# Kernel optimization log

Measured on AMD Instinct MI355X. Metric: run time of the kernel, lower is better.

Reference implementation:

```python
import jax, jax.numpy as jnp
import numpy as np

B, S, D = 2, 2048, 1024
H, HKV, HD = 16, 4, 64
FF = 4096
WINDOW = 1024
EPS = 1e-6


def _rope_tables(seq_len, head_dim, base=10000.0):
    inv_freq = 1.0 / (base ** (np.arange(0, head_dim, 2, dtype=np.float32) / head_dim))
    t = np.arange(seq_len, dtype=np.float32)
    freqs = np.outer(t, inv_freq)                       # [S, HD/2]
    emb = np.concatenate([freqs, freqs], axis=-1)       # [S, HD]
    return jnp.asarray(np.cos(emb)), jnp.asarray(np.sin(emb))


def setup_inputs() -> dict:
    key = jax.random.key(0)
    ks = jax.random.split(key, 16)
    s = lambda fan: 1.0 / np.sqrt(fan)
    cos, sin = _rope_tables(S, HD)
    return {
        "hidden_states": jax.random.normal(ks[0], (B, S, D), jnp.float32),
        "cos": cos, "sin": sin,
        "wq": jax.random.normal(ks[1], (D, H * HD), jnp.float32) * s(D),
        "bq": jnp.zeros((H * HD,), jnp.float32),
        "wk": jax.random.normal(ks[2], (D, HKV * HD), jnp.float32) * s(D),
        "bk": jnp.zeros((HKV * HD,), jnp.float32),
        "wv": jax.random.normal(ks[3], (D, HKV * HD), jnp.float32) * s(D),
        "bv": jnp.zeros((HKV * HD,), jnp.float32),
        "wo": jax.random.normal(ks[4], (H * HD, D), jnp.float32) * s(H * HD),
        "ln1_w": jnp.ones((D,), jnp.float32),
        "ln2_w": jnp.ones((D,), jnp.float32),
        "w_gate": jax.random.normal(ks[5], (D, FF), jnp.float32) * s(D),
        "w_up": jax.random.normal(ks[6], (D, FF), jnp.float32) * s(D),
        "w_down": jax.random.normal(ks[7], (FF, D), jnp.float32) * s(FF),
    }


def _rmsnorm(x, w, eps=EPS):
    var = jnp.mean(x.astype(jnp.float32) ** 2, axis=-1, keepdims=True)
    return (x * jax.lax.rsqrt(var + eps)).astype(x.dtype) * w


def _rotate_half(x):
    x1, x2 = jnp.split(x, 2, axis=-1)
    return jnp.concatenate([-x2, x1], axis=-1)


def reference(hidden_states, cos, sin, wq, bq, wk, bk, wv, bv, wo,
              ln1_w, ln2_w, w_gate, w_up, w_down):
    residual = hidden_states
    h = _rmsnorm(hidden_states, ln1_w)

    # projections -> [B, S, H, HD]
    q = (h @ wq + bq).reshape(B, S, H, HD)
    k = (h @ wk + bk).reshape(B, S, HKV, HD)
    v = (h @ wv + bv).reshape(B, S, HKV, HD)

    # RoPE
    c = cos[None, :, None, :]
    sn = sin[None, :, None, :]
    q = q * c + _rotate_half(q) * sn
    k = k * c + _rotate_half(k) * sn

    # GQA: repeat KV heads to H heads
    groups = H // HKV
    k = jnp.repeat(k, groups, axis=2)  # [B, S, H, HD]
    v = jnp.repeat(v, groups, axis=2)

    # sliding-window causal attention (flex_attention block-mask semantics)
    scale = 1.0 / np.sqrt(HD)
    scores = jnp.einsum("bqhd,bkhd->bhqk", q, k) * scale  # [B, H, S, S]
    i = jnp.arange(S)[:, None]
    j = jnp.arange(S)[None, :]
    mask = (j <= i) & (i - j < WINDOW)
    scores = jnp.where(mask[None, None], scores, jnp.finfo(scores.dtype).min)
    attn = jax.nn.softmax(scores, axis=-1)
    ctx = jnp.einsum("bhqk,bkhd->bqhd", attn, v).reshape(B, S, H * HD)

    h = residual + ctx @ wo

    residual2 = h
    h2 = _rmsnorm(h, ln2_w)
    mlp = (jax.nn.silu(h2 @ w_gate) * (h2 @ w_up)) @ w_down
    return residual2 + mlp
```

## Files before the change

kernel.cpp:

```cpp
#include <hip/hip_runtime.h>
#include <hip/hip_bf16.h>
#include <hip/hip_fp16.h>
#include <math.h>

#define BB 2
#define SS 2048
#define DD 1024
#define HH 16
#define HKVN 4
#define HDIM 64
#define FFD 4096
#define WND 1024
#define EPSF 1e-6f

typedef _Float16 f16;
typedef _Float16 half8 __attribute__((ext_vector_type(8)));
typedef float f32x4 __attribute__((ext_vector_type(4)));
typedef unsigned int u32;

#define GLOAD_LDS(gp, lp)                                                  \
  __builtin_amdgcn_global_load_lds(                                        \
      (const __attribute__((address_space(1))) u32*)(gp),                  \
      (__attribute__((address_space(3))) u32*)(lp), 16, 0, 0)

static __device__ inline u32 pack2(float a, float b) {
  unsigned short ua = __builtin_bit_cast(unsigned short, (f16)a);
  unsigned short ub = __builtin_bit_cast(unsigned short, (f16)b);
  return (u32)ua | ((u32)ub << 16);
}

__global__ __launch_bounds__(256) void prep_weights_kernel(
    const float* __restrict__ wq, const float* __restrict__ wk,
    const float* __restrict__ wv, const float* __restrict__ wo,
    const float* __restrict__ wg, const float* __restrict__ wu,
    const float* __restrict__ wd, const float* __restrict__ bq,
    const float* __restrict__ bk, const float* __restrict__ bv,
    f16* __restrict__ qkvT, f16* __restrict__ woT, f16* __restrict__ Wi,
    f16* __restrict__ wdT, float* __restrict__ biasC) {
  int t = blockIdx.x;
  if (t >= 3712) {
    int i = (t - 3712) * 256 + threadIdx.x;
    if (i < 1024)
      biasC[i] = bq[i];
    else if (i < 1280)
      biasC[i] = bk[i - 1024];
    else if (i < 1536)
      biasC[i] = bv[i - 1280];
    return;
  }
  const float* W;
  f16* Wt;
  int K, N, lt, rmul = 1, radd = 0;
  if (t < 256) {
    W = wq; Wt = qkvT; K = 1024; N = 1024; lt = t;
  } else if (t < 320) {
    W = wk; Wt = qkvT + (size_t)1024 * 1024; K = 1024; N = 256; lt = t - 256;
  } else if (t < 384) {
    W = wv; Wt = qkvT + (size_t)1280 * 1024; K = 1024; N = 256; lt = t - 320;
  } else if (t < 640) {
    W = wo; Wt = woT; K = 1024; N = 1024; lt = t - 384;
  } else if (t < 1664) {
    W = wg; Wt = Wi; K = 1024; N = 4096; lt = t - 640; rmul = 2; radd = 0;
  } else if (t < 2688) {
    W = wu; Wt = Wi; K = 1024; N = 4096; lt = t - 1664; rmul = 2; radd = 1;
  } else {
    W = wd; Wt = wdT; K = 4096; N = 1024; lt = t - 2688;
  }
  int ntx = N >> 6;
  int n0 = (lt % ntx) * 64, k0 = (lt / ntx) * 64;
  __shared__ float tile[64][65];
  int tx = threadIdx.x & 63, tr = threadIdx.x >> 6;
#pragma unroll
  for (int i = 0; i < 16; i++) {
    int r = tr + i * 4;
    tile[r][tx] = W[(size_t)(k0 + r) * N + n0 + tx];
  }
  __syncthreads();
  int kx = (threadIdx.x & 31) * 2;
  int rr = threadIdx.x >> 5;
#pragma unroll
  for (int i = 0; i < 8; i++) {
    int r = rr + i * 8;
    u32 w = pack2(tile[kx][r], tile[kx + 1][r]);
    *(u32*)(Wt + ((size_t)((n0 + r) * rmul + radd)) * K + k0 + kx) = w;
  }
}

__global__ __launch_bounds__(256) void rmsnorm_kernel(
    const float* __restrict__ x, const float* __restrict__ w,
    f16* __restrict__ out) {
  int row = blockIdx.x;
  int tid = threadIdx.x;
  float4 v = ((const float4*)(x + (size_t)row * 1024))[tid];
  float ss = v.x * v.x + v.y * v.y + v.z * v.z + v.w * v.w;
  for (int o = 32; o > 0; o >>= 1) ss += __shfl_down(ss, o, 64);
  __shared__ float red[4];
  int wid = tid >> 6, lane = tid & 63;
  if (lane == 0) red[wid] = ss;
  __syncthreads();
  if (tid == 0)
    red[0] = rsqrtf((red[0] + red[1] + red[2] + red[3]) / 1024.f + EPSF);
  __syncthreads();
  float rs = red[0];
  float4 wv = ((const float4*)w)[tid];
  u32 lo = pack2(v.x * rs * wv.x, v.y * rs * wv.y);
  u32 hi = pack2(v.z * rs * wv.z, v.w * rs * wv.w);
  *(int2*)(out + (size_t)row * 1024 + tid * 4) = make_int2((int)lo, (int)hi);
}

__global__ __launch_bounds__(256) void qkv_gemm(
    const f16* __restrict__ A, const f16* __restrict__ Bt,
    const float* __restrict__ biasC, const float* __restrict__ cos_t,
    const float* __restrict__ sin_t, f16* __restrict__ Qh,
    f16* __restrict__ Kh, f16* __restrict__ Vh, int M, int N, int K) {
  __shared__ __align__(16) char smem[3 * 16384];
  const int tid = threadIdx.x;
  const int lane = tid & 63;
  const int wid = tid >> 6;
  const int wr = wid >> 1, wc = wid & 1;
  const int row0 = blockIdx.y * 128, col0 = blockIdx.x * 128;

  f32x4 acc[4][4];
#pragma unroll
  for (int m = 0; m < 4; m++)
#pragma unroll
    for (int n = 0; n < 4; n++) acc[m][n] = (f32x4){0.f, 0.f, 0.f, 0.f};

  auto stage = [&](int buf, int k0) {
    char* base = smem + buf * 16384;
#pragma unroll
    for (int q = 0; q < 2; q++) {
      int s = wid * 128 + q * 64 + lane;
      int r = s >> 2;
      int cg = (s & 3) ^ ((r >> 1) & 3);
      size_t goff = (size_t)r * K + k0 + cg * 8;
      u32 ldsb = (u32)((wid * 2 + q) * 1024);
      GLOAD_LDS(A + (size_t)row0 * K + goff, base + ldsb);
      GLOAD_LDS(Bt + (size_t)col0 * K + goff, base + 8192 + ldsb);
    }
  };
  auto off = [&](int r, int g) -> int {
    return r * 64 + ((g ^ ((r >> 1) & 3)) << 4);
  };

  const int nt = K / 32;
  stage(0, 0);
  if (nt > 1) stage(1, 32);
  int cur = 0;
  const int g = lane >> 4, l15 = lane & 15;
  for (int t = 0; t < nt; t++) {
    if (t + 1 < nt)
      asm volatile("s_waitcnt vmcnt(4)" ::: "memory");
    else
      asm volatile("s_waitcnt vmcnt(0)" ::: "memory");
    asm volatile("s_waitcnt lgkmcnt(0)" ::: "memory");
    __builtin_amdgcn_sched_barrier(0);
    __builtin_amdgcn_s_barrier();
    __builtin_amdgcn_sched_barrier(0);
    const char* base = smem + cur * 16384;
    half8 af[4], bf[4];
#pragma unroll
    for (int m = 0; m < 4; m++) {
      int r = wr * 64 + m * 16 + l15;
      af[m] = *(const half8*)(base + off(r, g));
    }
#pragma unroll
    for (int n = 0; n < 4; n++) {
      int c = wc * 64 + n * 16 + l15;
      bf[n] = *(const half8*)(base + 8192 + off(c, g));
    }
    if (t + 2 < nt) {
      int nb = cur + 2;
      if (nb >= 3) nb -= 3;
      stage(nb, (t + 2) * 32);
    }
    __builtin_amdgcn_s_setprio(1);
#pragma unroll
    for (int m = 0; m < 4; m++)
#pragma unroll
      for (int n = 0; n < 4; n++)
        acc[m][n] =
            __builtin_amdgcn_mfma_f32_16x16x32_f16(af[m], bf[n], acc[m][n], 0, 0, 0);
    __builtin_amdgcn_s_setprio(0);
    cur = (cur + 1 == 3) ? 0 : cur + 1;
  }

  const int typ = (col0 < 1024) ? 0 : (col0 < 1280 ? 1 : 2);
#pragma unroll
  for (int m = 0; m < 4; m++) {
#pragma unroll
    for (int v = 0; v < 4; v++) {
      int r = row0 + wr * 64 + m * 16 + (lane >> 4) * 4 + v;
      int s = r & (SS - 1);
      if (typ == 2) {
#pragma unroll
        for (int n = 0; n < 4; n++) {
          int c = col0 + wc * 64 + n * 16 + l15;
          float vv = acc[m][n][v] + biasC[c];
          Vh[(size_t)r * 256 + (c - 1280)] = (f16)vv;
        }
      } else {
#pragma unroll
        for (int n = 0; n < 2; n++) {
          int d = n * 16 + l15;
          int c1 = col0 + wc * 64 + d;
          float x1 = acc[m][n][v] + biasC[c1];
          float x2 = acc[m][n + 2][v] + biasC[c1 + 32];
          float cv = cos_t[s * HDIM + d];
          float sv = sin_t[s * HDIM + d];
          float o1 = x1 * cv - x2 * sv;
          float o2 = x2 * cv + x1 * sv;
          if (typ == 0) {
            int h = c1 >> 6;
            f16* qp = Qh + ((size_t)r * HH + h) * HDIM + d;
            qp[0] = (f16)(o1 * 0.125f);
            qp[32] = (f16)(o2 * 0.125f);
          } else {
            int hk = (c1 - 1024) >> 6;
            f16* kp = Kh + ((size_t)r * HKVN + hk) * HDIM + d;
            kp[0] = (f16)o1;
            kp[32] = (f16)o2;
          }
        }
      }
    }
  }
}

__global__ __launch_bounds__(256) void gemm_n64(
    const f16* __restrict__ A, const f16* __restrict__ Bt,
    const float* __restrict__ resid, float* __restrict__ Cf, int M, int N,
    int K) {
  __shared__ __align__(16) char smem[3 * 12288];
  const int tid = threadIdx.x;
  const int lane = tid & 63;
  const int wid = tid >> 6;
  const int wr = wid >> 1, wc = wid & 1;
  const int row0 = blockIdx.y * 128, col0 = blockIdx.x * 64;

  f32x4 acc[4][2];
#pragma unroll
  for (int m = 0; m < 4; m++)
#pragma unroll
    for (int n = 0; n < 2; n++) acc[m][n] = (f32x4){0.f, 0.f, 0.f, 0.f};

  auto stage = [&](int buf, int k0) {
    char* base = smem + buf * 12288;
#pragma unroll
    for (int p = 0; p < 2; p++) {
      int s = p * 256 + tid;
      int r = s >> 2;
      int cg = (s & 3) ^ ((r >> 1) & 3);
      size_t goff = (size_t)r * K + k0 + cg * 8;
      GLOAD_LDS(A + (size_t)row0 * K + goff, base + p * 4096 + wid * 1024);
    }
    {
      int s = tid;
      int r = s >> 2;
      int cg = (s & 3) ^ ((r >> 1) & 3);
      size_t goff = (size_t)r * K + k0 + cg * 8;
      GLOAD_LDS(Bt + (size_t)col0 * K + goff, base + 8192 + wid * 1024);
    }
  };
  auto off = [&](int r, int g) -> int {
    return r * 64 + ((g ^ ((r >> 1) & 3)) << 4);
  };

  const int nt = K / 32;
  stage(0, 0);
  if (nt > 1) stage(1, 32);
  int cur = 0;
  const int g = lane >> 4, l15 = lane & 15;
  for (int t = 0; t < nt; t++) {
    if (t + 1 < nt)
      asm volatile("s_waitcnt vmcnt(3)" ::: "memory");
    else
      asm volatile("s_waitcnt vmcnt(0)" ::: "memory");
    asm volatile("s_waitcnt lgkmcnt(0)" ::: "memory");
    __builtin_amdgcn_sched_barrier(0);
    __builtin_amdgcn_s_barrier();
    __builtin_amdgcn_sched_barrier(0);
    const char* base = smem + cur * 12288;
    half8 af[4], bf[2];
#pragma unroll
    for (int m = 0; m < 4; m++) {
      int r = wr * 64 + m * 16 + l15;
      af[m] = *(const half8*)(base + off(r, g));
    }
#pragma unroll
    for (int n = 0; n < 2; n++) {
      int c = wc * 32 + n * 16 + l15;
      bf[n] = *(const half8*)(base + 8192 + off(c, g));
    }
    if (t + 2 < nt) {
      int nb = cur + 2;
      if (nb >= 3) nb -= 3;
      stage(nb, (t + 2) * 32);
    }
    __builtin_amdgcn_s_setprio(1);
#pragma unroll
    for (int m = 0; m < 4; m++)
#pragma unroll
      for (int n = 0; n < 2; n++)
        acc[m][n] =
            __builtin_amdgcn_mfma_f32_16x16x32_f16(af[m], bf[n], acc[m][n], 0, 0, 0);
    __builtin_amdgcn_s_setprio(0);
    cur = (cur + 1 == 3) ? 0 : cur + 1;
  }

#pragma unroll
  for (int m = 0; m < 4; m++) {
#pragma unroll
    for (int n = 0; n < 2; n++) {
#pragma unroll
      for (int v = 0; v < 4; v++) {
        int r = row0 + wr * 64 + m * 16 + (lane >> 4) * 4 + v;
        int c = col0 + wc * 32 + n * 16 + l15;
        float vv = acc[m][n][v] + resid[(size_t)r * N + c];
        Cf[(size_t)r * N + c] = vv;
      }
    }
  }
}

__global__ __launch_bounds__(512) void gateup_gemm8(
    const f16* __restrict__ A, const f16* __restrict__ Wi,
    f16* __restrict__ ACT, int M) {
  __shared__ __align__(16) char smem[2 * 65536];
  const int tid = threadIdx.x;
  const int lane = tid & 63;
  const int wid = tid >> 6;
  const int wr = wid >> 2;
  const int wc = wid & 3;
  const int l15 = lane & 15, g = lane >> 4;
  const int row0 = blockIdx.y * 256, col0 = blockIdx.x * 256;
  const int K = 1024;

  f32x4 acc[8][4];
#pragma unroll
  for (int m = 0; m < 8; m++)
#pragma unroll
    for (int n = 0; n < 4; n++) acc[m][n] = (f32x4){0.f, 0.f, 0.f, 0.f};

  const f16* Ap = A + (size_t)row0 * K;
  const f16* Bp = Wi + (size_t)col0 * K;

  auto stage = [&](const f16* src, char* dstbase, int kt) {
    int k0 = kt * 64;
#pragma unroll
    for (int p = 0; p < 4; p++) {
      int slot = p * 512 + tid;
      int r = slot >> 3, c = slot & 7;
      int cc = c ^ (r & 7);
      GLOAD_LDS(src + (size_t)r * K + k0 + cc * 8,
                dstbase + p * 8192 + wid * 1024);
    }
  };

  stage(Ap, smem, 0);
  stage(Bp, smem + 32768, 0);
  stage(Bp, smem + 65536 + 32768, 1);
  asm volatile("s_waitcnt vmcnt(4)" ::: "memory");
  __builtin_amdgcn_sched_barrier(0);
  __builtin_amdgcn_s_barrier();
  __builtin_amdgcn_sched_barrier(0);

  for (int i = 0; i < 8; i++) {
    const bool last = (i == 7);
#pragma unroll
    for (int half = 0; half < 2; half++) {
      const char* tb = smem + half * 65536;
      half8 bf[4][2];
#pragma unroll
      for (int q = 0; q < 4; q++) {
        int m0 = 2 * q, m1 = 2 * q + 1;
        int r0 = wr * 128 + m0 * 16 + l15;
        int r1 = wr * 128 + m1 * 16 + l15;
        half8 a0 = *(const half8*)(tb + r0 * 128 + ((g ^ (r0 & 7)) << 4));
        half8 a1 = *(const half8*)(tb + r0 * 128 + (((4 + g) ^ (r0 & 7)) << 4));
        half8 a2 = *(const half8*)(tb + r1 * 128 + ((g ^ (r1 & 7)) << 4));
        half8 a3 = *(const half8*)(tb + r1 * 128 + (((4 + g) ^ (r1 & 7)) << 4));
        if (q == 0) {
#pragma unroll
          for (int n = 0; n < 4; n++) {
            int rb = wc * 64 + n * 16 + l15;
            bf[n][0] =
                *(const half8*)(tb + 32768 + rb * 128 + ((g ^ (rb & 7)) << 4));
            bf[n][1] = *(const half8*)(tb + 32768 + rb * 128 +
                                       (((4 + g) ^ (rb & 7)) << 4));
          }
        }
        if (half == 0) {
          if (q == 0) stage(Ap, smem + 65536, 2 * i + 1);
          if (q == 2 && !last) stage(Bp, smem + 32768, 2 * i + 2);
        } else {
          if (q == 0 && !last) stage(Ap, smem, 2 * i + 2);
          if (q == 2 && !last)
            stage(Bp, smem + 65536 + 32768, 2 * i + 3);
        }
        __builtin_amdgcn_sched_barrier(0);
        __builtin_amdgcn_s_barrier();
        asm volatile("s_waitcnt lgkmcnt(0)" ::: "memory");
        __builtin_amdgcn_sched_barrier(0);
        __builtin_amdgcn_s_setprio(1);
#pragma unroll
        for (int n = 0; n < 4; n++) {
          acc[m0][n] =
              __builtin_amdgcn_mfma_f32_16x16x32_f16(a0, bf[n][0], acc[m0][n], 0, 0, 0);
          acc[m0][n] =
              __builtin_amdgcn_mfma_f32_16x16x32_f16(a1, bf[n][1], acc[m0][n], 0, 0, 0);
          acc[m1][n] =
              __builtin_amdgcn_mfma_f32_16x16x32_f16(a2, bf[n][0], acc[m1][n], 0, 0, 0);
          acc[m1][n] =
              __builtin_amdgcn_mfma_f32_16x16x32_f16(a3, bf[n][1], acc[m1][n], 0, 0, 0);
        }
        __builtin_amdgcn_s_setprio(0);
        if (q == 3) {
          if (half == 0) {
            if (last)
              asm volatile("s_waitcnt vmcnt(0)" ::: "memory");
            else
              asm volatile("s_waitcnt vmcnt(4)" ::: "memory");
          } else if (!last) {
            asm volatile("s_waitcnt vmcnt(4)" ::: "memory");
          }
        }
        __builtin_amdgcn_sched_barrier(0);
        __builtin_amdgcn_s_barrier();
        __builtin_amdgcn_sched_barrier(0);
      }
    }
  }

  const int col0h = col0 >> 1;
#pragma unroll
  for (int m = 0; m < 8; m++) {
#pragma unroll
    for (int n = 0; n < 4; n++) {
#pragma unroll
      for (int v = 0; v < 4; v++) {
        float other = __shfl_xor(acc[m][n][v], 1, 64);
        if (!(l15 & 1)) {
          float gg = acc[m][n][v];
          float sv = gg / (1.f + __expf(-gg));
          int r = row0 + wr * 128 + m * 16 + g * 4 + v;
          int c = col0h + wc * 32 + n * 8 + (l15 >> 1);
          ACT[(size_t)r * FFD + c] = (f16)(sv * other);
        }
      }
    }
  }
}

__global__ __launch_bounds__(256) void vtrans_kernel(
    const f16* __restrict__ Vh, f16* __restrict__ Vt) {
  __shared__ f16 tile[64][72];
  int st = blockIdx.x & 31;
  int hk = (blockIdx.x >> 5) & 3;
  int b = blockIdx.x >> 7;
  int s0 = st * 64;
  int tid = threadIdx.x;
  int r = tid >> 2, cg = tid & 3;
#pragma unroll
  for (int i = 0; i < 2; i++) {
    const f16* src =
        Vh + (size_t)(b * SS + s0 + r) * 256 + hk * HDIM + cg * 16 + i * 8;
    *(int4*)&tile[r][cg * 16 + i * 8] = *(const int4*)src;
  }
  __syncthreads();
  int dd = tid >> 2, sg = tid & 3;
#pragma unroll
  for (int i = 0; i < 4; i++) {
    int c0 = sg * 16 + i * 4;
    unsigned short a0 = __builtin_bit_cast(unsigned short, tile[c0 + 0][dd]);
    unsigned short a1 = __builtin_bit_cast(unsigned short, tile[c0 + 1][dd]);
    unsigned short a2 = __builtin_bit_cast(unsigned short, tile[c0 + 2][dd]);
    unsigned short a3 = __builtin_bit_cast(unsigned short, tile[c0 + 3][dd]);
    u32 w0 = (u32)a0 | ((u32)a1 << 16);
    u32 w1 = (u32)a2 | ((u32)a3 << 16);
    *(int2*)(Vt + ((size_t)(b * HKVN + hk) * HDIM + dd) * SS + s0 + c0) =
        make_int2((int)w0, (int)w1);
  }
}

__global__ __launch_bounds__(256) void attn_kernel(
    const f16* __restrict__ Qh, const f16* __restrict__ Kh,
    const f16* __restrict__ Vt, f16* __restrict__ O) {
  __shared__ __align__(16) char smem[2 * 16384 + 4 * 4608];
  const int tid = threadIdx.x;
  const int lane = tid & 63;
  const int wid = tid >> 6;
  const int l15 = lane & 15;
  const int g = lane >> 4;
  int qt = blockIdx.x & 63;
  int hk = (blockIdx.x >> 6) & 3;
  int b = blockIdx.x >> 8;
  int s0 = qt * 32;
  int h = hk * 4 + wid;

  half8 qf[2][2];
#pragma unroll
  for (int n = 0; n < 2; n++) {
    int q = s0 + n * 16 + l15;
    const f16* qp = Qh + (((size_t)b * SS + q) * HH + h) * HDIM;
#pragma unroll
    for (int kk = 0; kk < 2; kk++) qf[n][kk] = *(const half8*)(qp + kk * 32 + g * 8);
  }

  const int tb = (s0 >= WND) ? ((s0 - (WND - 1)) >> 6) : 0;
  const int te = (s0 + 31) >> 6;

  f32x4 acc_o[2][4];
#pragma unroll
  for (int m2 = 0; m2 < 2; m2++)
#pragma unroll
    for (int n = 0; n < 4; n++) acc_o[m2][n] = (f32x4){0.f, 0.f, 0.f, 0.f};
  float mrun[2] = {-1e30f, -1e30f};
  float lrun[2] = {0.f, 0.f};

  char* pw = smem + 32768 + wid * 4608;

  auto stage = [&](int buf, int tt) {
    int jt0 = tt * 64;
    char* kbase = smem + buf * 16384;
#pragma unroll
    for (int q2 = 0; q2 < 2; q2++) {
      int slot = (wid * 2 + q2) * 64 + lane;
      int r = slot >> 3, c = slot & 7;
      int cc = c ^ (r & 7);
      u32 ldsb = (u32)((wid * 2 + q2) * 1024);
      const f16* gk =
          Kh + ((size_t)(b * SS + jt0 + r) * HKVN + hk) * HDIM + cc * 8;
      GLOAD_LDS(gk, kbase + ldsb);
      const f16* gv =
          Vt + ((size_t)(b * HKVN + hk) * HDIM + r) * SS + jt0 + cc * 8;
      GLOAD_LDS(gv, kbase + 8192 + ldsb);
    }
  };

  stage(0, tb);
  __syncthreads();
  for (int tt = tb; tt <= te; tt++) {
    int buf = (tt - tb) & 1;
    if (tt < te) stage(buf ^ 1, tt + 1);
    const char* kb = smem + buf * 16384;
    const char* vbp = kb + 8192;
    int jt0 = tt * 64;

    f32x4 acc_s[4][2];
#pragma unroll
    for (int m = 0; m < 4; m++)
#pragma unroll
      for (int n = 0; n < 2; n++) acc_s[m][n] = (f32x4){0.f, 0.f, 0.f, 0.f};
#pragma unroll
    for (int kk = 0; kk < 2; kk++) {
      half8 af[4];
#pragma unroll
      for (int m = 0; m < 4; m++) {
        int key = m * 16 + l15;
        af[m] = *(const half8*)(kb + key * 128 + (((kk * 4 + g) ^ (key & 7)) << 4));
      }
#pragma unroll
      for (int m = 0; m < 4; m++)
#pragma unroll
        for (int n = 0; n < 2; n++)
          acc_s[m][n] = __builtin_amdgcn_mfma_f32_16x16x32_f16(af[m], qf[n][kk],
                                                               acc_s[m][n], 0, 0, 0);
    }

    float tmax[2] = {-1e38f, -1e38f};
#pragma unroll
    for (int m = 0; m < 4; m++)
#pragma unroll
      for (int n = 0; n < 2; n++)
#pragma unroll
        for (int v = 0; v < 4; v++) {
          int j = jt0 + m * 16 + g * 4 + v;
          int q = s0 + n * 16 + l15;
          float s = acc_s[m][n][v];
          s = ((unsigned)(q - j) < (unsigned)WND) ? s : -1e38f;
          acc_s[m][n][v] = s;
          tmax[n] = fmaxf(tmax[n], s);
        }
#pragma unroll
    for (int n = 0; n < 2; n++) {
      tmax[n] = fmaxf(tmax[n], __shfl_xor(tmax[n], 16, 64));
      tmax[n] = fmaxf(tmax[n], __shfl_xor(tmax[n], 32, 64));
    }
    float corr[2], rs[2];
#pragma unroll
    for (int n = 0; n < 2; n++) {
      float mn = fmaxf(mrun[n], tmax[n]);
      corr[n] = __expf(mrun[n] - mn);
      mrun[n] = mn;
      rs[n] = 0.f;
    }
#pragma unroll
    for (int m = 0; m < 4; m++)
#pragma unroll
      for (int n = 0; n < 2; n++) {
        float p0 = __expf(acc_s[m][n][0] - mrun[n]);
        float p1 = __expf(acc_s[m][n][1] - mrun[n]);
        float p2 = __expf(acc_s[m][n][2] - mrun[n]);
        float p3 = __expf(acc_s[m][n][3] - mrun[n]);
        rs[n] += (p0 + p1) + (p2 + p3);
        *(int2*)(pw + (n * 16 + l15) * 144 + (m * 16 + g * 4) * 2) =
            make_int2((int)pack2(p0, p1), (int)pack2(p2, p3));
      }
#pragma unroll
    for (int n = 0; n < 2; n++) {
      rs[n] += __shfl_xor(rs[n], 16, 64);
      rs[n] += __shfl_xor(rs[n], 32, 64);
      lrun[n] = lrun[n] * corr[n] + rs[n];
    }
#pragma unroll
    for (int m2 = 0; m2 < 2; m2++)
#pragma unroll
      for (int v = 0; v < 4; v++) {
        float cw = __shfl(corr[m2], g * 4 + v, 64);
#pragma unroll
        for (int n = 0; n < 4; n++) acc_o[m2][n][v] *= cw;
      }
#pragma unroll
    for (int kk = 0; kk < 2; kk++) {
      half8 ap[2], vf[4];
#pragma unroll
      for (int m2 = 0; m2 < 2; m2++)
        ap[m2] = *(const half8*)(pw + (m2 * 16 + l15) * 144 + (kk * 32 + g * 8) * 2);
#pragma unroll
      for (int n = 0; n < 4; n++) {
        int d = n * 16 + l15;
        vf[n] = *(const half8*)(vbp + d * 128 + (((kk * 4 + g) ^ (d & 7)) << 4));
      }
#pragma unroll
      for (int m2 = 0; m2 < 2; m2++)
#pragma unroll
        for (int n = 0; n < 4; n++)
          acc_o[m2][n] = __builtin_amdgcn_mfma_f32_16x16x32_f16(ap[m2], vf[n],
                                                                acc_o[m2][n], 0, 0, 0);
    }
    __syncthreads();
  }

#pragma unroll
  for (int m2 = 0; m2 < 2; m2++)
#pragma unroll
    for (int v = 0; v < 4; v++) {
      float li = __shfl(lrun[m2], g * 4 + v, 64);
      float inv = 1.f / li;
      int q = s0 + m2 * 16 + g * 4 + v;
#pragma unroll
      for (int n = 0; n < 4; n++) {
        int d = n * 16 + l15;
        O[(((size_t)b * SS + q) * HH + h) * HDIM + d] =
            (f16)(acc_o[m2][n][v] * inv);
      }
    }
}

extern "C" void kernel_launch(void* const* d_in, const int* in_sizes, int n_in,
                              void* d_out, int out_size, void* d_ws,
                              size_t ws_size, hipStream_t stream) {
  const float* hidden = (const float*)d_in[0];
  const float* cos_t = (const float*)d_in[1];
  const float* sin_t = (const float*)d_in[2];
  const float* wq = (const float*)d_in[3];
  const float* bq = (const float*)d_in[4];
  const float* wk = (const float*)d_in[5];
  const float* bk = (const float*)d_in[6];
  const float* wv = (const float*)d_in[7];
  const float* bv = (const float*)d_in[8];
  const float* wo = (const float*)d_in[9];
  const float* ln1 = (const float*)d_in[10];
  const float* ln2 = (const float*)d_in[11];
  const float* wg = (const float*)d_in[12];
  const float* wu = (const float*)d_in[13];
  const float* wd = (const float*)d_in[14];
  float* out = (float*)d_out;
  char* ws = (char*)d_ws;

  const int M = BB * SS;

  f16* qkvT = (f16*)ws;
  f16* woT = (f16*)(ws + (3u << 20));
  f16* Wi = (f16*)(ws + (5u << 20));
  f16* wdT = (f16*)(ws + (21u << 20));
  f16* Anh = (f16*)(ws + (29u << 20));
  f16* CTXh = (f16*)(ws + (37u << 20));
  f16* Vh = (f16*)(ws + (45u << 20));
  f16* Qh = (f16*)(ws + (57u << 20));
  f16* Kh = (f16*)(ws + (65u << 20));
  f16* Vt = (f16*)(ws + (67u << 20));
  f16* ACTh = (f16*)(ws + (45u << 20));
  float* biasC = (float*)(ws + (81u << 20));

  prep_weights_kernel<<<3718, 256, 0, stream>>>(wq, wk, wv, wo, wg, wu, wd, bq,
                                                bk, bv, qkvT, woT, Wi, wdT,
                                                biasC);
  rmsnorm_kernel<<<M, 256, 0, stream>>>(hidden, ln1, Anh);
  qkv_gemm<<<dim3(1536 / 128, M / 128), 256, 0, stream>>>(
      Anh, qkvT, biasC, cos_t, sin_t, Qh, Kh, Vh, M, 1536, DD);
  vtrans_kernel<<<BB * HKVN * (SS / 64), 256, 0, stream>>>(Vh, Vt);
  attn_kernel<<<BB * HKVN * (SS / 32), 256, 0, stream>>>(Qh, Kh, Vt, CTXh);
  gemm_n64<<<dim3(DD / 64, M / 128), 256, 0, stream>>>(CTXh, woT, hidden, out,
                                                       M, DD, DD);
  rmsnorm_kernel<<<M, 256, 0, stream>>>(out, ln2, Anh);
  gateup_gemm8<<<dim3(2 * FFD / 256, M / 256), 512, 0, stream>>>(Anh, Wi, ACTh,
                                                                 M);
  gemm_n64<<<dim3(DD / 64, M / 128), 256, 0, stream>>>(ACTh, wdT, out, out, M,
                                                       DD, FFD);
}
```

Measured before the change: 269.4 us.

## Fuse first RMSNorm into weight prep, use exp2 softmax with lazy rescale, split staging

Folds the first RMSNorm into the weight-preparation launch as extra blocks, removing one kernel launch. Q is prescaled by log2(e) so attention uses exp2f, and the running-max rescale of the output accumulator is skipped when no row's max grows by more than a threshold (conditional rescaling). The gate/up GEMM now issues its global-to-LDS loads in half-tiles spread across more q-steps to smooth memory traffic. The lazy rescale lets probabilities exceed 1 by up to 2^11 before being stored as fp16, which adds some risk to range and accuracy.

```diff
diff --git a/kernel.cpp b/kernel.cpp
--- a/kernel.cpp
+++ b/kernel.cpp
@@ -36,8 +36,30 @@
     const float* __restrict__ wd, const float* __restrict__ bq,
     const float* __restrict__ bk, const float* __restrict__ bv,
     f16* __restrict__ qkvT, f16* __restrict__ woT, f16* __restrict__ Wi,
-    f16* __restrict__ wdT, float* __restrict__ biasC) {
+    f16* __restrict__ wdT, float* __restrict__ biasC,
+    const float* __restrict__ hidden, const float* __restrict__ ln1,
+    f16* __restrict__ Anh) {
   int t = blockIdx.x;
+  if (t >= 3718) {
+    int row = t - 3718;
+    int tid = threadIdx.x;
+    float4 v = ((const float4*)(hidden + (size_t)row * 1024))[tid];
+    float ss = v.x * v.x + v.y * v.y + v.z * v.z + v.w * v.w;
+    for (int o = 32; o > 0; o >>= 1) ss += __shfl_down(ss, o, 64);
+    __shared__ float red[4];
+    int wid = tid >> 6, lane = tid & 63;
+    if (lane == 0) red[wid] = ss;
+    __syncthreads();
+    if (tid == 0)
+      red[0] = rsqrtf((red[0] + red[1] + red[2] + red[3]) / 1024.f + EPSF);
+    __syncthreads();
+    float rs = red[0];
+    float4 wv4 = ((const float4*)ln1)[tid];
+    u32 lo = pack2(v.x * rs * wv4.x, v.y * rs * wv4.y);
+    u32 hi = pack2(v.z * rs * wv4.z, v.w * rs * wv4.w);
+    *(int2*)(Anh + (size_t)row * 1024 + tid * 4) = make_int2((int)lo, (int)hi);
+    return;
+  }
   if (t >= 3712) {
     int i = (t - 3712) * 256 + threadIdx.x;
     if (i < 1024)
@@ -186,6 +208,7 @@
   }
 
   const int typ = (col0 < 1024) ? 0 : (col0 < 1280 ? 1 : 2);
+  const float QSC = 0.125f * 1.4426950408889634f;
 #pragma unroll
   for (int m = 0; m < 4; m++) {
 #pragma unroll
@@ -213,8 +236,8 @@
           if (typ == 0) {
             int h = c1 >> 6;
             f16* qp = Qh + ((size_t)r * HH + h) * HDIM + d;
-            qp[0] = (f16)(o1 * 0.125f);
-            qp[32] = (f16)(o2 * 0.125f);
+            qp[0] = (f16)(o1 * QSC);
+            qp[32] = (f16)(o2 * QSC);
           } else {
             int hk = (c1 - 1024) >> 6;
             f16* kp = Kh + ((size_t)r * HKVN + hk) * HDIM + d;
@@ -345,21 +368,25 @@
   const f16* Ap = A + (size_t)row0 * K;
   const f16* Bp = Wi + (size_t)col0 * K;
 
-  auto stage = [&](const f16* src, char* dstbase, int kt) {
+  auto stageH = [&](const f16* src, char* dst, int kt, int h) {
     int k0 = kt * 64;
 #pragma unroll
-    for (int p = 0; p < 4; p++) {
+    for (int p = 0; p < 2; p++) {
       int slot = p * 512 + tid;
-      int r = slot >> 3, c = slot & 7;
+      int r = (slot >> 3) + h * 128;
+      int c = slot & 7;
       int cc = c ^ (r & 7);
       GLOAD_LDS(src + (size_t)r * K + k0 + cc * 8,
-                dstbase + p * 8192 + wid * 1024);
+                dst + h * 16384 + p * 8192 + wid * 1024);
     }
   };
 
-  stage(Ap, smem, 0);
-  stage(Bp, smem + 32768, 0);
-  stage(Bp, smem + 65536 + 32768, 1);
+  stageH(Ap, smem, 0, 0);
+  stageH(Ap, smem, 0, 1);
+  stageH(Bp, smem + 32768, 0, 0);
+  stageH(Bp, smem + 32768, 0, 1);
+  stageH(Bp, smem + 65536 + 32768, 1, 0);
+  stageH(Bp, smem + 65536 + 32768, 1, 1);
   asm volatile("s_waitcnt vmcnt(4)" ::: "memory");
   __builtin_amdgcn_sched_barrier(0);
   __builtin_amdgcn_s_barrier();
@@ -375,7 +402,7 @@
       for (int q = 0; q < 4; q++) {
         int m0 = 2 * q, m1 = 2 * q + 1;
         int r0 = wr * 128 + m0 * 16 + l15;
-        int r1 = wr * 128 + m1 * 16 + l15;
+        int r1 = r0 + 16;
         half8 a0 = *(const half8*)(tb + r0 * 128 + ((g ^ (r0 & 7)) << 4));
         half8 a1 = *(const half8*)(tb + r0 * 128 + (((4 + g) ^ (r0 & 7)) << 4));
         half8 a2 = *(const half8*)(tb + r1 * 128 + ((g ^ (r1 & 7)) << 4));
@@ -391,12 +418,25 @@
           }
         }
         if (half == 0) {
-          if (q == 0) stage(Ap, smem + 65536, 2 * i + 1);
-          if (q == 2 && !last) stage(Bp, smem + 32768, 2 * i + 2);
+          if (q == 0)
+            stageH(Ap, smem + 65536, 2 * i + 1, 0);
+          else if (q == 1)
+            stageH(Ap, smem + 65536, 2 * i + 1, 1);
+          else if (q == 2) {
+            if (!last) stageH(Bp, smem + 32768, 2 * i + 2, 0);
+          } else {
+            if (!last) stageH(Bp, smem + 32768, 2 * i + 2, 1);
+          }
         } else {
-          if (q == 0 && !last) stage(Ap, smem, 2 * i + 2);
-          if (q == 2 && !last)
-            stage(Bp, smem + 65536 + 32768, 2 * i + 3);
+          if (q == 0) {
+            if (!last) stageH(Ap, smem, 2 * i + 2, 0);
+          } else if (q == 1) {
+            if (!last) stageH(Ap, smem, 2 * i + 2, 1);
+          } else if (q == 2) {
+            if (!last) stageH(Bp, smem + 65536 + 32768, 2 * i + 3, 0);
+          } else {
+            if (!last) stageH(Bp, smem + 65536 + 32768, 2 * i + 3, 1);
+          }
         }
         __builtin_amdgcn_sched_barrier(0);
         __builtin_amdgcn_s_barrier();
@@ -588,21 +628,29 @@
       tmax[n] = fmaxf(tmax[n], __shfl_xor(tmax[n], 32, 64));
     }
     float corr[2], rs[2];
-#pragma unroll
-    for (int n = 0; n < 2; n++) {
-      float mn = fmaxf(mrun[n], tmax[n]);
-      corr[n] = __expf(mrun[n] - mn);
-      mrun[n] = mn;
-      rs[n] = 0.f;
-    }
+    bool skip = __all((tmax[0] <= mrun[0] + 11.0f) &&
+                      (tmax[1] <= mrun[1] + 11.0f));
+    if (skip) {
+      corr[0] = 1.f;
+      corr[1] = 1.f;
+    } else {
+#pragma unroll
+      for (int n = 0; n < 2; n++) {
+        float mn = fmaxf(mrun[n], tmax[n]);
+        corr[n] = exp2f(mrun[n] - mn);
+        mrun[n] = mn;
+      }
+    }
+    rs[0] = 0.f;
+    rs[1] = 0.f;
 #pragma unroll
     for (int m = 0; m < 4; m++)
 #pragma unroll
       for (int n = 0; n < 2; n++) {
-        float p0 = __expf(acc_s[m][n][0] - mrun[n]);
-        float p1 = __expf(acc_s[m][n][1] - mrun[n]);
-        float p2 = __expf(acc_s[m][n][2] - mrun[n]);
-        float p3 = __expf(acc_s[m][n][3] - mrun[n]);
+        float p0 = exp2f(acc_s[m][n][0] - mrun[n]);
+        float p1 = exp2f(acc_s[m][n][1] - mrun[n]);
+        float p2 = exp2f(acc_s[m][n][2] - mrun[n]);
+        float p3 = exp2f(acc_s[m][n][3] - mrun[n]);
         rs[n] += (p0 + p1) + (p2 + p3);
         *(int2*)(pw + (n * 16 + l15) * 144 + (m * 16 + g * 4) * 2) =
             make_int2((int)pack2(p0, p1), (int)pack2(p2, p3));
@@ -613,14 +661,16 @@
       rs[n] += __shfl_xor(rs[n], 32, 64);
       lrun[n] = lrun[n] * corr[n] + rs[n];
     }
-#pragma unroll
-    for (int m2 = 0; m2 < 2; m2++)
-#pragma unroll
-      for (int v = 0; v < 4; v++) {
-        float cw = __shfl(corr[m2], g * 4 + v, 64);
-#pragma unroll
-        for (int n = 0; n < 4; n++) acc_o[m2][n][v] *= cw;
-      }
+    if (!skip) {
+#pragma unroll
+      for (int m2 = 0; m2 < 2; m2++)
+#pragma unroll
+        for (int v = 0; v < 4; v++) {
+          float cw = __shfl(corr[m2], g * 4 + v, 64);
+#pragma unroll
+          for (int n = 0; n < 4; n++) acc_o[m2][n][v] *= cw;
+        }
+    }
 #pragma unroll
     for (int kk = 0; kk < 2; kk++) {
       half8 ap[2], vf[4];
@@ -694,10 +744,9 @@
   f16* ACTh = (f16*)(ws + (45u << 20));
   float* biasC = (float*)(ws + (81u << 20));
 
-  prep_weights_kernel<<<3718, 256, 0, stream>>>(wq, wk, wv, wo, wg, wu, wd, bq,
-                                                bk, bv, qkvT, woT, Wi, wdT,
-                                                biasC);
-  rmsnorm_kernel<<<M, 256, 0, stream>>>(hidden, ln1, Anh);
+  prep_weights_kernel<<<3718 + M, 256, 0, stream>>>(
+      wq, wk, wv, wo, wg, wu, wd, bq, bk, bv, qkvT, woT, Wi, wdT, biasC,
+      hidden, ln1, Anh);
   qkv_gemm<<<dim3(1536 / 128, M / 128), 256, 0, stream>>>(
       Anh, qkvT, biasC, cos_t, sin_t, Qh, Kh, Vh, M, 1536, DD);
   vtrans_kernel<<<BB * HKVN * (SS / 64), 256, 0, stream>>>(Vh, Vt);
```

New measurement: 272.8 us. Within noise of the previous version (+1.3%).
